# Kernel optimization log

Hardware: AMD Instinct MI355X
Metric: run time of the kernel (lower is better)

The kernel has to match this reference:

```python
import jax, jax.numpy as jnp
import numpy as np

N, E, D, H, ED = 50000, 600000, 128, 2, 5
C = D // H  # per-head channels = 64


def _lin(k, fan_in, fan_out):
    return jax.random.normal(k, (fan_out, fan_in), jnp.float32) / np.sqrt(fan_in)


def setup_inputs() -> dict:
    key = jax.random.key(0)
    ks = jax.random.split(key, 12)
    return {
        "x": jax.random.normal(ks[0], (N, D), jnp.float32),
        "edge_index": jax.random.randint(ks[1], (2, E), 0, N, dtype=jnp.int32),
        "edge_attr": jax.random.normal(ks[2], (E, ED), jnp.float32),
        "Wq": _lin(ks[3], D, D), "bq": jnp.zeros((D,), jnp.float32),
        "Wk": _lin(ks[4], D, D), "bk": jnp.zeros((D,), jnp.float32),
        "Wv": _lin(ks[5], D, D), "bv": jnp.zeros((D,), jnp.float32),
        "We": _lin(ks[6], ED, D),                       # lin_edge, bias=False in PyG
        "Wskip": _lin(ks[7], D, D), "bskip": jnp.zeros((D,), jnp.float32),
        "Wbeta": _lin(ks[8], 3 * D, 1),                 # lin_beta, bias=False
        "Wproj": _lin(ks[9], D, D), "bproj": jnp.zeros((D,), jnp.float32),
    }


def reference(x, edge_index, edge_attr, Wq, bq, Wk, bk, Wv, bv, We,
              Wskip, bskip, Wbeta, Wproj, bproj):
    src, dst = edge_index[0], edge_index[1]
    # node projections -> [N, H, C]
    q = (x @ Wq.T + bq).reshape(N, H, C)
    k = (x @ Wk.T + bk).reshape(N, H, C)
    v = (x @ Wv.T + bv).reshape(N, H, C)
    e = (edge_attr @ We.T).reshape(E, H, C)
    # gather per-edge, fold in edge features
    kj = k[src] + e                                   # [E, H, C]
    vj = v[src] + e                                   # [E, H, C]
    alpha = (q[dst] * kj).sum(-1) / np.sqrt(C)        # [E, H]
    # segment softmax over edges grouped by dst node
    amax = jax.ops.segment_max(alpha, dst, num_segments=N)   # [N, H]
    ex = jnp.exp(alpha - amax[dst])
    denom = jax.ops.segment_sum(ex, dst, num_segments=N)     # [N, H]
    w = ex / denom[dst]                               # [E, H]
    # scatter-aggregate weighted values, concat heads
    out = jax.ops.segment_sum(vj * w[:, :, None], dst, num_segments=N).reshape(N, D)
    # beta-gated skip connection
    x_r = x @ Wskip.T + bskip
    beta = jax.nn.sigmoid(jnp.concatenate([out, x_r, out - x_r], axis=-1) @ Wbeta.T)  # [N,1]
    out = beta * x_r + (1.0 - beta) * out
    # outer projection (dropout is identity in eval)
    return out @ Wproj.T + bproj
```

## Files before the change

kernel.cpp:

```cpp
#include <hip/hip_runtime.h>
#include <stdint.h>
#include <math.h>

#define D 128
#define EDIM 5

typedef __attribute__((ext_vector_type(8))) short bf16x8;
typedef __attribute__((ext_vector_type(4))) float f32x4;

__device__ __forceinline__ ushort f2b(float f) {
  union { float f; uint u; } v; v.f = f;
  uint u = v.u;
  return (ushort)((u + 0x7fff + ((u >> 16) & 1)) >> 16);
}
__device__ __forceinline__ float blo(uint u) {
  union { uint u; float f; } v; v.u = u << 16; return v.f;
}
__device__ __forceinline__ float bhi(uint u) {
  union { uint u; float f; } v; v.u = u & 0xffff0000u; return v.f;
}


__global__ void zero_int_kernel(int* __restrict__ p, int n) {
  int i = blockIdx.x * blockDim.x + threadIdx.x;
  if (i < n) p[i] = 0;
}

__global__ void hist_kernel(const int* __restrict__ ei, int* __restrict__ deg, int E) {
  int e = blockIdx.x * blockDim.x + threadIdx.x;
  if (e < E) atomicAdd(&deg[ei[(size_t)E + e]], 1);
}

__global__ __launch_bounds__(256) void scan_p1(const int* __restrict__ deg,
                                               int* __restrict__ off,
                                               int* __restrict__ blockSum, int n4) {
  __shared__ int waveTot[4];
  int idx = blockIdx.x * 256 + threadIdx.x;
  int4 v = make_int4(0, 0, 0, 0);
  if (idx < n4) v = ((const int4*)deg)[idx];
  int c0 = v.x, c1 = c0 + v.y, c2 = c1 + v.z, c3 = c2 + v.w;
  int tot = c3;
  int lane = threadIdx.x & 63, w = threadIdx.x >> 6;
  int incl = tot;
#pragma unroll
  for (int ofs = 1; ofs < 64; ofs <<= 1) {
    int t = __shfl_up(incl, ofs, 64);
    if (lane >= ofs) incl += t;
  }
  if (lane == 63) waveTot[w] = incl;
  __syncthreads();
  int wbase = 0;
  for (int i = 0; i < w; ++i) wbase += waveTot[i];
  int excl = wbase + incl - tot;
  if (idx < n4) {
    int4 o;
    o.x = excl; o.y = excl + c0; o.z = excl + c1; o.w = excl + c2;
    ((int4*)off)[idx] = o;
  }
  if (threadIdx.x == 255) blockSum[blockIdx.x] = wbase + incl;
}

__global__ void scan_p2(const int* __restrict__ blockSum, int* __restrict__ blockBase,
                        int* __restrict__ off_last, int nb) {
  int lane = threadIdx.x;
  int v = (lane < nb) ? blockSum[lane] : 0;
  int incl = v;
#pragma unroll
  for (int ofs = 1; ofs < 64; ofs <<= 1) {
    int t = __shfl_up(incl, ofs, 64);
    if (lane >= ofs) incl += t;
  }
  if (lane < nb) blockBase[lane] = incl - v;
  if (lane == 63) *off_last = incl;
}

__global__ __launch_bounds__(256) void scan_p3(int* __restrict__ off,
                                               const int* __restrict__ blockBase,
                                               int* __restrict__ cursor, int n4) {
  int idx = blockIdx.x * 256 + threadIdx.x;
  if (idx >= n4) return;
  int b = blockBase[blockIdx.x];
  int4 v = ((int4*)off)[idx];
  v.x += b; v.y += b; v.z += b; v.w += b;
  ((int4*)off)[idx] = v;
  ((int4*)cursor)[idx] = make_int4(0, 0, 0, 0);
}

__global__ void scatter_kernel(const int* __restrict__ ei, const float* __restrict__ ea,
                               const int* __restrict__ off, int* __restrict__ cursor,
                               int* __restrict__ ssrc, uint4* __restrict__ easrt, int E) {
  int e = blockIdx.x * blockDim.x + threadIdx.x;
  if (e >= E) return;
  int dst = ei[(size_t)E + e];
  int pos = off[dst] + atomicAdd(&cursor[dst], 1);
  ssrc[pos] = ei[e];
  const float* p = ea + (size_t)e * EDIM;
  uint e0 = f2b(p[0]), e1 = f2b(p[1]), e2 = f2b(p[2]), e3 = f2b(p[3]), e4 = f2b(p[4]);
  easrt[pos] = make_uint4(e0 | (e1 << 16), e2 | (e3 << 16), e4, 0);
}

__global__ void cvt_w_kernel(const float* __restrict__ Wq, const float* __restrict__ Wk,
                             const float* __restrict__ Wv, const float* __restrict__ Wr,
                             const float* __restrict__ bq, const float* __restrict__ bk,
                             const float* __restrict__ bv, const float* __restrict__ br,
                             const float* __restrict__ We, const float* __restrict__ Wp,
                             ushort* __restrict__ Wcat, float* __restrict__ bcat,
                             ushort* __restrict__ Wpb) {
  int i = blockIdx.x * blockDim.x + threadIdx.x;
  if (i < 512 * D) {
    int r = i >> 7;
    float v;
    if (r < 128)      v = Wq[i] * 0.125f;
    else if (r < 256) v = Wk[i - 128 * D];
    else if (r < 384) v = Wv[i - 256 * D];
    else              v = Wr[i - 384 * D];
    Wcat[i] = f2b(v);
  } else if (i < 512 * D + 128 * D) {
    int ie = i - 512 * D;
    int r = ie >> 7, c = ie & 127;
    int h = r >> 3, j = r & 7;
    float v = 0.f;
    if (h < 2 && j < 5) {
      for (int d = 0; d < 64; ++d) {
        int dd = h * 64 + d;
        v += We[(size_t)dd * EDIM + j] * 0.125f * Wq[(size_t)dd * D + c];
      }
    }
    Wcat[(size_t)(512 + r) * D + c] = f2b(v);
  }
  if (i < D * D) Wpb[i] = f2b(Wp[i]);
  if (i < 512) {
    float v = (i < 128) ? bq[i] * 0.125f
            : (i < 256) ? bk[i - 128]
            : (i < 384) ? bv[i - 256] : br[i - 384];
    bcat[i] = v;
  } else if (i < 640) {
    int t = i - 512;
    int h = t >> 3, j = t & 7;
    float v = 0.f;
    if (h < 2 && j < 5) {
      for (int d = 0; d < 64; ++d) {
        int dd = h * 64 + d;
        v += bq[dd] * 0.125f * We[(size_t)dd * EDIM + j];
      }
    }
    bcat[i] = v;
  }
}

__global__ __launch_bounds__(256) void proj_gemm_kernel(
    const float* __restrict__ x, const ushort* __restrict__ Wcat,
    const float* __restrict__ bcat,
    ushort* __restrict__ q, ushort* __restrict__ kv, ushort* __restrict__ xr,
    float* __restrict__ qwe, int M)
{
  __shared__ __attribute__((aligned(16))) ushort As[64][128];
  __shared__ __attribute__((aligned(16))) ushort Bs[128][128];
  const int tid = threadIdx.x;
  const int rowBase = blockIdx.x * 64;

#pragma unroll
  for (int it = 0; it < 4; ++it) {
    int i = it * 256 + tid;
    int r = i >> 4, c = i & 15;
    int gr = rowBase + r;
    float4 a0 = make_float4(0.f, 0.f, 0.f, 0.f), a1 = a0;
    if (gr < M) {
      a0 = *(const float4*)(x + (size_t)gr * D + c * 8);
      a1 = *(const float4*)(x + (size_t)gr * D + c * 8 + 4);
    }
    uint4 w;
    w.x = (uint)f2b(a0.x) | ((uint)f2b(a0.y) << 16);
    w.y = (uint)f2b(a0.z) | ((uint)f2b(a0.w) << 16);
    w.z = (uint)f2b(a1.x) | ((uint)f2b(a1.y) << 16);
    w.w = (uint)f2b(a1.z) | ((uint)f2b(a1.w) << 16);
    *(uint4*)(&As[r][(c ^ (r & 7)) * 8]) = w;
  }

  const int lane = tid & 63;
  const int wave = tid >> 6;
  const int wm = (wave >> 1) * 32;
  const int wn = (wave & 1) * 64;
  const int lrow = lane & 15;
  const int kgrp = lane >> 4;
  const int orow = (lane >> 4) * 4;
  const int ocol = lane & 15;

  for (int cb = 0; cb < 5; ++cb) {
#pragma unroll
    for (int it = 0; it < 8; ++it) {
      int i = it * 256 + tid;
      int r = i >> 4, c = i & 15;
      uint4 bv4 = *(const uint4*)(Wcat + (size_t)(cb * 128 + r) * D + c * 8);
      *(uint4*)(&Bs[r][(c ^ (r & 7)) * 8]) = bv4;
    }
    __syncthreads();

    f32x4 acc[2][4] = {};
#pragma unroll
    for (int ks = 0; ks < 4; ++ks) {
      int chunk = ks * 4 + kgrp;
      bf16x8 a[2], b[4];
#pragma unroll
      for (int m = 0; m < 2; ++m) {
        int r = wm + m * 16 + lrow;
        a[m] = *(const bf16x8*)&As[r][(chunk ^ (r & 7)) * 8];
      }
#pragma unroll
      for (int n = 0; n < 4; ++n) {
        int r = wn + n * 16 + lrow;
        b[n] = *(const bf16x8*)&Bs[r][(chunk ^ (r & 7)) * 8];
      }
#pragma unroll
      for (int m = 0; m < 2; ++m)
#pragma unroll
        for (int n = 0; n < 4; ++n)
          acc[m][n] = __builtin_amdgcn_mfma_f32_16x16x32_bf16(a[m], b[n], acc[m][n], 0, 0, 0);
    }

#pragma unroll
    for (int m = 0; m < 2; ++m) {
#pragma unroll
      for (int n = 0; n < 4; ++n) {
        int col = cb * 128 + wn + n * 16 + ocol;
        float bi = bcat[col];
        int sel = col >> 7, c = col & 127;
#pragma unroll
        for (int ii = 0; ii < 4; ++ii) {
          int gr = rowBase + wm + m * 16 + orow + ii;
          if (gr >= M) continue;
          float v = acc[m][n][ii] + bi;
          if (sel == 0)      q[(size_t)gr * D + c] = f2b(v);
          else if (sel == 1) kv[(size_t)gr * 2 * D + c] = f2b(v);
          else if (sel == 2) kv[(size_t)gr * 2 * D + D + c] = f2b(v);
          else if (sel == 3) xr[(size_t)gr * D + c] = f2b(v);
          else if (c < 16)   qwe[(size_t)gr * 16 + c] = v;
        }
      }
    }
    __syncthreads();
  }
}

__global__ __launch_bounds__(256) void out_gemm_kernel(
    const ushort* __restrict__ g, const ushort* __restrict__ Wpb,
    const float* __restrict__ bp, float* __restrict__ out, int M)
{
  __shared__ __attribute__((aligned(16))) ushort As[64][128];
  __shared__ __attribute__((aligned(16))) ushort Bs[128][128];
  const int tid = threadIdx.x;
  const int rowBase = blockIdx.x * 64;

#pragma unroll
  for (int it = 0; it < 4; ++it) {
    int i = it * 256 + tid;
    int r = i >> 4, c = i & 15;
    int gr = rowBase + r;
    uint4 av = make_uint4(0, 0, 0, 0);
    if (gr < M) av = *(const uint4*)(g + (size_t)gr * D + c * 8);
    *(uint4*)(&As[r][(c ^ (r & 7)) * 8]) = av;
  }
#pragma unroll
  for (int it = 0; it < 8; ++it) {
    int i = it * 256 + tid;
    int r = i >> 4, c = i & 15;
    uint4 bv4 = *(const uint4*)(Wpb + (size_t)r * D + c * 8);
    *(uint4*)(&Bs[r][(c ^ (r & 7)) * 8]) = bv4;
  }
  __syncthreads();

  const int lane = tid & 63;
  const int wave = tid >> 6;
  const int wm = (wave >> 1) * 32;
  const int wn = (wave & 1) * 64;
  const int lrow = lane & 15;
  const int kgrp = lane >> 4;

  f32x4 acc[2][4] = {};
#pragma unroll
  for (int ks = 0; ks < 4; ++ks) {
    int chunk = ks * 4 + kgrp;
    bf16x8 a[2], b[4];
#pragma unroll
    for (int m = 0; m < 2; ++m) {
      int r = wm + m * 16 + lrow;
      a[m] = *(const bf16x8*)&As[r][(chunk ^ (r & 7)) * 8];
    }
#pragma unroll
    for (int n = 0; n < 4; ++n) {
      int r = wn + n * 16 + lrow;
      b[n] = *(const bf16x8*)&Bs[r][(chunk ^ (r & 7)) * 8];
    }
#pragma unroll
    for (int m = 0; m < 2; ++m)
#pragma unroll
      for (int n = 0; n < 4; ++n)
        acc[m][n] = __builtin_amdgcn_mfma_f32_16x16x32_bf16(a[m], b[n], acc[m][n], 0, 0, 0);
  }

  const int orow = (lane >> 4) * 4;
  const int ocol = lane & 15;
#pragma unroll
  for (int m = 0; m < 2; ++m) {
#pragma unroll
    for (int n = 0; n < 4; ++n) {
      int col = wn + n * 16 + ocol;
      float bi = bp[col];
#pragma unroll
      for (int ii = 0; ii < 4; ++ii) {
        int gr = rowBase + wm + m * 16 + orow + ii;
        if (gr >= M) continue;
        out[(size_t)gr * D + col] = acc[m][n][ii] + bi;
      }
    }
  }
}

__global__ __launch_bounds__(256) void node_attn_kernel(
    const ushort* __restrict__ q, const ushort* __restrict__ kv,
    const ushort* __restrict__ xr, ushort* __restrict__ g,
    const float* __restrict__ qwe, const uint4* __restrict__ easrt,
    const float* __restrict__ We, const float* __restrict__ Wb,
    const int* __restrict__ off, const int* __restrict__ ssrc, int N)
{
  const int wid = threadIdx.x >> 6;
  const int lane = threadIdx.x & 63;
  const int node = blockIdx.x * 4 + wid;
  if (node >= N) return;
  const int grp = lane >> 4;
  const int i = lane & 15;
  const int di = i * 8;
  const int head = i >> 3;

  float qr[8];
  {
    uint4 qa = *(const uint4*)(q + (size_t)node * D + di);
    qr[0] = blo(qa.x); qr[1] = bhi(qa.x); qr[2] = blo(qa.y); qr[3] = bhi(qa.y);
    qr[4] = blo(qa.z); qr[5] = bhi(qa.z); qr[6] = blo(qa.w); qr[7] = bhi(qa.w);
  }
  float qw[5];
  {
    const float* qp = qwe + (size_t)node * 16 + head * 8;
    float4 t = *(const float4*)qp;
    qw[0] = t.x; qw[1] = t.y; qw[2] = t.z; qw[3] = t.w; qw[4] = qp[4];
  }

  const int beg = off[node], end = off[node + 1];
  float m = -INFINITY, s = 0.f;
  float o[8] = {0.f, 0.f, 0.f, 0.f, 0.f, 0.f, 0.f, 0.f};
  float wea[5] = {0.f, 0.f, 0.f, 0.f, 0.f};

  if (beg < end) {
    int p0 = beg + grp;
    bool valid_c = p0 < end;
    int pl = valid_c ? p0 : beg;
    int src_c = ssrc[pl];
    uint4 eau_c = easrt[pl];
    const ushort* kp0 = kv + (size_t)src_c * (2 * D);
    uint4 ku_c = *(const uint4*)(kp0 + di);
    uint4 vu_c = *(const uint4*)(kp0 + D + di);

    for (int pb = beg; pb < end; pb += 4) {
      int pn = pb + 4 + grp;
      bool valid_n = pn < end;
      int pln = valid_n ? pn : pl;
      int src_n = ssrc[pln];
      uint4 eau_n = easrt[pln];

      float ea0 = blo(eau_c.x), ea1 = bhi(eau_c.x), ea2 = blo(eau_c.y),
            ea3 = bhi(eau_c.y), ea4 = blo(eau_c.z);
      float part = qr[0] * blo(ku_c.x) + qr[1] * bhi(ku_c.x)
                 + qr[2] * blo(ku_c.y) + qr[3] * bhi(ku_c.y)
                 + qr[4] * blo(ku_c.z) + qr[5] * bhi(ku_c.z)
                 + qr[6] * blo(ku_c.w) + qr[7] * bhi(ku_c.w);
#pragma unroll
      for (int ofs = 1; ofs < 8; ofs <<= 1) part += __shfl_xor(part, ofs, 64);
      float eadot = qw[0] * ea0 + qw[1] * ea1 + qw[2] * ea2 + qw[3] * ea3 + qw[4] * ea4;
      float alpha = valid_c ? (part + eadot) : -INFINITY;

      const ushort* kpn = kv + (size_t)src_n * (2 * D);
      uint4 ku_n = *(const uint4*)(kpn + di);
      uint4 vu_n = *(const uint4*)(kpn + D + di);

      float v0 = blo(vu_c.x), v1 = bhi(vu_c.x), v2 = blo(vu_c.y), v3 = bhi(vu_c.y),
            v4 = blo(vu_c.z), v5 = bhi(vu_c.z), v6 = blo(vu_c.w), v7 = bhi(vu_c.w);

      if (__any(alpha > m + 8.f)) {
        float nm = fmaxf(m, alpha);
        float scale = (m > -1e30f) ? __expf(m - nm) : 0.f;
        float pw = (alpha > -1e30f) ? __expf(alpha - nm) : 0.f;
        m = nm;
        s = s * scale + pw;
        o[0] = o[0] * scale + pw * v0; o[1] = o[1] * scale + pw * v1;
        o[2] = o[2] * scale + pw * v2; o[3] = o[3] * scale + pw * v3;
        o[4] = o[4] * scale + pw * v4; o[5] = o[5] * scale + pw * v5;
        o[6] = o[6] * scale + pw * v6; o[7] = o[7] * scale + pw * v7;
        wea[0] = wea[0] * scale + pw * ea0; wea[1] = wea[1] * scale + pw * ea1;
        wea[2] = wea[2] * scale + pw * ea2; wea[3] = wea[3] * scale + pw * ea3;
        wea[4] = wea[4] * scale + pw * ea4;
      } else {
        float pw = (alpha > -1e30f) ? __expf(alpha - m) : 0.f;
        s += pw;
        o[0] += pw * v0; o[1] += pw * v1; o[2] += pw * v2; o[3] += pw * v3;
        o[4] += pw * v4; o[5] += pw * v5; o[6] += pw * v6; o[7] += pw * v7;
        wea[0] += pw * ea0; wea[1] += pw * ea1; wea[2] += pw * ea2;
        wea[3] += pw * ea3; wea[4] += pw * ea4;
      }

      ku_c = ku_n; vu_c = vu_n; eau_c = eau_n; valid_c = valid_n; pl = pln;
    }
  }

#pragma unroll
  for (int ofs = 16; ofs < 64; ofs <<= 1) {
    float m2 = __shfl_xor(m, ofs, 64);
    float s2 = __shfl_xor(s, ofs, 64);
    float o2[8], w2[5];
#pragma unroll
    for (int j = 0; j < 8; ++j) o2[j] = __shfl_xor(o[j], ofs, 64);
#pragma unroll
    for (int j = 0; j < 5; ++j) w2[j] = __shfl_xor(wea[j], ofs, 64);
    float nm = fmaxf(m, m2);
    float e1 = (m > -1e30f) ? __expf(m - nm) : 0.f;
    float e2 = (m2 > -1e30f) ? __expf(m2 - nm) : 0.f;
    s = s * e1 + s2 * e2;
#pragma unroll
    for (int j = 0; j < 8; ++j) o[j] = o[j] * e1 + o2[j] * e2;
#pragma unroll
    for (int j = 0; j < 5; ++j) wea[j] = wea[j] * e1 + w2[j] * e2;
    m = nm;
  }

  float inv = (s > 0.f) ? (1.f / s) : 0.f;
#pragma unroll
  for (int j = 0; j < 8; ++j) o[j] *= inv;
#pragma unroll
  for (int j = 0; j < 5; ++j) wea[j] *= inv;

  {
    const float* wp = We + (size_t)di * EDIM;
    float4 w[10];
#pragma unroll
    for (int t = 0; t < 10; ++t) w[t] = *(const float4*)(wp + 4 * t);
#pragma unroll
    for (int r = 0; r < 8; ++r)
#pragma unroll
      for (int j = 0; j < 5; ++j) {
        int idx = r * 5 + j;
        o[r] += wea[j] * ((const float*)&w[idx >> 2])[idx & 3];
      }
  }

  float xrv[8];
  {
    uint4 xa = *(const uint4*)(xr + (size_t)node * D + di);
    xrv[0] = blo(xa.x); xrv[1] = bhi(xa.x); xrv[2] = blo(xa.y); xrv[3] = bhi(xa.y);
    xrv[4] = blo(xa.z); xrv[5] = bhi(xa.z); xrv[6] = blo(xa.w); xrv[7] = bhi(xa.w);
  }
  float part = 0.f;
#pragma unroll
  for (int r = 0; r < 8; ++r) {
    float w1 = Wb[di + r] + Wb[256 + di + r];
    float w2 = Wb[128 + di + r] - Wb[256 + di + r];
    part += o[r] * w1 + xrv[r] * w2;
  }
#pragma unroll
  for (int ofs = 1; ofs < 16; ofs <<= 1) part += __shfl_xor(part, ofs, 64);
  float beta = 1.f / (1.f + __expf(-part));

  if (grp == 0) {
    uint pk[4];
#pragma unroll
    for (int r = 0; r < 4; ++r) {
      float g0 = beta * xrv[2 * r] + (1.f - beta) * o[2 * r];
      float g1 = beta * xrv[2 * r + 1] + (1.f - beta) * o[2 * r + 1];
      pk[r] = (uint)f2b(g0) | ((uint)f2b(g1) << 16);
    }
    *(uint4*)(g + (size_t)node * D + di) = make_uint4(pk[0], pk[1], pk[2], pk[3]);
  }
}


extern "C" void kernel_launch(void* const* d_in, const int* in_sizes, int n_in,
                              void* d_out, int out_size, void* d_ws, size_t ws_size,
                              hipStream_t stream)
{
  const float* x  = (const float*)d_in[0];
  const int*   ei = (const int*)d_in[1];
  const float* ea = (const float*)d_in[2];
  const float* Wq = (const float*)d_in[3];
  const float* bq = (const float*)d_in[4];
  const float* Wk = (const float*)d_in[5];
  const float* bk = (const float*)d_in[6];
  const float* Wv = (const float*)d_in[7];
  const float* bv = (const float*)d_in[8];
  const float* We = (const float*)d_in[9];
  const float* Wr = (const float*)d_in[10];
  const float* br = (const float*)d_in[11];
  const float* Wb = (const float*)d_in[12];
  const float* Wp = (const float*)d_in[13];
  const float* bp = (const float*)d_in[14];

  const int N = in_sizes[0] / D;
  const int E = in_sizes[1] / 2;
  float* out = (float*)d_out;

  char* ws = (char*)d_ws;
  size_t o = 0;
  auto alloc = [&](size_t bytes) -> void* {
    void* p = ws + o;
    o = (o + bytes + 255) & ~(size_t)255;
    return p;
  };
  ushort* q      = (ushort*)alloc((size_t)N * D * sizeof(ushort));
  ushort* kv     = (ushort*)alloc((size_t)N * 2 * D * sizeof(ushort));
  ushort* xr     = (ushort*)alloc((size_t)N * D * sizeof(ushort));
  ushort* g      = (ushort*)alloc((size_t)N * D * sizeof(ushort));
  float*  qwe    = (float*)alloc((size_t)N * 16 * sizeof(float));
  ushort* Wcat   = (ushort*)alloc((size_t)640 * D * sizeof(ushort));
  float*  bcat   = (float*)alloc(640 * sizeof(float));
  ushort* Wpb    = (ushort*)alloc((size_t)D * D * sizeof(ushort));
  int*    deg    = (int*)alloc((size_t)N * sizeof(int));
  int*    cursor = (int*)alloc((size_t)N * sizeof(int));
  int*    offs   = (int*)alloc((size_t)(N + 1) * sizeof(int));
  int*    ssrc   = (int*)alloc((size_t)E * sizeof(int));
  uint4*  easrt  = (uint4*)alloc((size_t)E * sizeof(uint4));
  int*    bsum   = (int*)alloc(64 * sizeof(int));
  int*    bbase  = (int*)alloc(64 * sizeof(int));

  const int n4 = N / 4;
  const int nb = (n4 + 255) / 256;

  zero_int_kernel<<<(N + 255) / 256, 256, 0, stream>>>(deg, N);
  hist_kernel<<<(E + 255) / 256, 256, 0, stream>>>(ei, deg, E);
  scan_p1<<<nb, 256, 0, stream>>>(deg, offs, bsum, n4);
  scan_p2<<<1, 64, 0, stream>>>(bsum, bbase, offs + N, nb);
  scan_p3<<<nb, 256, 0, stream>>>(offs, bbase, cursor, n4);
  scatter_kernel<<<(E + 255) / 256, 256, 0, stream>>>(ei, ea, offs, cursor, ssrc, easrt, E);

  cvt_w_kernel<<<(512 * D + 128 * D + 255) / 256, 256, 0, stream>>>(
      Wq, Wk, Wv, Wr, bq, bk, bv, br, We, Wp, Wcat, bcat, Wpb);

  proj_gemm_kernel<<<(N + 63) / 64, 256, 0, stream>>>(x, Wcat, bcat, q, kv, xr, qwe, N);

  node_attn_kernel<<<(N + 3) / 4, 256, 0, stream>>>(q, kv, xr, g, qwe, easrt, We, Wb,
                                                    offs, ssrc, N);

  out_gemm_kernel<<<(N + 63) / 64, 256, 0, stream>>>(g, Wpb, bp, out, N);
}
```

Baseline: 241.2 us.

## Pack src into edge record, deepen gather prefetch, use exp2, trim GEMM tail

The source index is now packed into the unused fourth word of the sorted edge-attribute record, which removes the separate ssrc array and one dependent load per edge. The attention loop is unrolled three ways with rotating registers, so K/V gathers are prefetched two groups ahead and edge records three ahead. The softmax switches to exp2 by folding log2(e) into the Q scale, and the rescale threshold is adjusted to match. Separately, the degree zeroing is folded into the weight-convert kernel, and the projection GEMM skips the unused columns of its last column block. The costs are higher register pressure in the attention kernel and more duplicated loads at the tail of each segment.

```diff
diff --git a/kernel.cpp b/kernel.cpp
--- a/kernel.cpp
+++ b/kernel.cpp
@@ -4,9 +4,14 @@
 
 #define D 128
 #define EDIM 5
+#define QSCALE 0.1803368801111204f
 
 typedef __attribute__((ext_vector_type(8))) short bf16x8;
 typedef __attribute__((ext_vector_type(4))) float f32x4;
+
+__device__ __forceinline__ float fexp2(float x) {
+  return __builtin_amdgcn_exp2f(x);
+}
 
 __device__ __forceinline__ ushort f2b(float f) {
   union { float f; uint u; } v; v.f = f;
@@ -20,11 +25,6 @@
   union { uint u; float f; } v; v.u = u & 0xffff0000u; return v.f;
 }
 
-
-__global__ void zero_int_kernel(int* __restrict__ p, int n) {
-  int i = blockIdx.x * blockDim.x + threadIdx.x;
-  if (i < n) p[i] = 0;
-}
 
 __global__ void hist_kernel(const int* __restrict__ ei, int* __restrict__ deg, int E) {
   int e = blockIdx.x * blockDim.x + threadIdx.x;
@@ -88,15 +88,14 @@
 
 __global__ void scatter_kernel(const int* __restrict__ ei, const float* __restrict__ ea,
                                const int* __restrict__ off, int* __restrict__ cursor,
-                               int* __restrict__ ssrc, uint4* __restrict__ easrt, int E) {
+                               uint4* __restrict__ easrt, int E) {
   int e = blockIdx.x * blockDim.x + threadIdx.x;
   if (e >= E) return;
   int dst = ei[(size_t)E + e];
   int pos = off[dst] + atomicAdd(&cursor[dst], 1);
-  ssrc[pos] = ei[e];
   const float* p = ea + (size_t)e * EDIM;
   uint e0 = f2b(p[0]), e1 = f2b(p[1]), e2 = f2b(p[2]), e3 = f2b(p[3]), e4 = f2b(p[4]);
-  easrt[pos] = make_uint4(e0 | (e1 << 16), e2 | (e3 << 16), e4, 0);
+  easrt[pos] = make_uint4(e0 | (e1 << 16), e2 | (e3 << 16), e4, (uint)ei[e]);
 }
 
 __global__ void cvt_w_kernel(const float* __restrict__ Wq, const float* __restrict__ Wk,
@@ -105,12 +104,13 @@
                              const float* __restrict__ bv, const float* __restrict__ br,
                              const float* __restrict__ We, const float* __restrict__ Wp,
                              ushort* __restrict__ Wcat, float* __restrict__ bcat,
-                             ushort* __restrict__ Wpb) {
+                             ushort* __restrict__ Wpb, int* __restrict__ deg, int N) {
   int i = blockIdx.x * blockDim.x + threadIdx.x;
+  if (i < N) deg[i] = 0;
   if (i < 512 * D) {
     int r = i >> 7;
     float v;
-    if (r < 128)      v = Wq[i] * 0.125f;
+    if (r < 128)      v = Wq[i] * QSCALE;
     else if (r < 256) v = Wk[i - 128 * D];
     else if (r < 384) v = Wv[i - 256 * D];
     else              v = Wr[i - 384 * D];
@@ -123,14 +123,14 @@
     if (h < 2 && j < 5) {
       for (int d = 0; d < 64; ++d) {
         int dd = h * 64 + d;
-        v += We[(size_t)dd * EDIM + j] * 0.125f * Wq[(size_t)dd * D + c];
+        v += We[(size_t)dd * EDIM + j] * QSCALE * Wq[(size_t)dd * D + c];
       }
     }
     Wcat[(size_t)(512 + r) * D + c] = f2b(v);
   }
   if (i < D * D) Wpb[i] = f2b(Wp[i]);
   if (i < 512) {
-    float v = (i < 128) ? bq[i] * 0.125f
+    float v = (i < 128) ? bq[i] * QSCALE
             : (i < 256) ? bk[i - 128]
             : (i < 384) ? bv[i - 256] : br[i - 384];
     bcat[i] = v;
@@ -141,7 +141,7 @@
     if (h < 2 && j < 5) {
       for (int d = 0; d < 64; ++d) {
         int dd = h * 64 + d;
-        v += bq[dd] * 0.125f * We[(size_t)dd * EDIM + j];
+        v += bq[dd] * QSCALE * We[(size_t)dd * EDIM + j];
       }
     }
     bcat[i] = v;
@@ -191,6 +191,7 @@
     for (int it = 0; it < 8; ++it) {
       int i = it * 256 + tid;
       int r = i >> 4, c = i & 15;
+      if (cb == 4 && r >= 16) continue;
       uint4 bv4 = *(const uint4*)(Wcat + (size_t)(cb * 128 + r) * D + c * 8);
       *(uint4*)(&Bs[r][(c ^ (r & 7)) * 8]) = bv4;
     }
@@ -214,14 +215,17 @@
 #pragma unroll
       for (int m = 0; m < 2; ++m)
 #pragma unroll
-        for (int n = 0; n < 4; ++n)
+        for (int n = 0; n < 4; ++n) {
+          if (cb == 4 && (wn + n * 16) >= 16) continue;
           acc[m][n] = __builtin_amdgcn_mfma_f32_16x16x32_bf16(a[m], b[n], acc[m][n], 0, 0, 0);
+        }
     }
 
 #pragma unroll
     for (int m = 0; m < 2; ++m) {
 #pragma unroll
       for (int n = 0; n < 4; ++n) {
+        if (cb == 4 && (wn + n * 16) >= 16) continue;
         int col = cb * 128 + wn + n * 16 + ocol;
         float bi = bcat[col];
         int sel = col >> 7, c = col & 127;
@@ -321,7 +325,7 @@
     const ushort* __restrict__ xr, ushort* __restrict__ g,
     const float* __restrict__ qwe, const uint4* __restrict__ easrt,
     const float* __restrict__ We, const float* __restrict__ Wb,
-    const int* __restrict__ off, const int* __restrict__ ssrc, int N)
+    const int* __restrict__ off, int N)
 {
   const int wid = threadIdx.x >> 6;
   const int lane = threadIdx.x & 63;
@@ -351,64 +355,74 @@
   float wea[5] = {0.f, 0.f, 0.f, 0.f, 0.f};
 
   if (beg < end) {
-    int p0 = beg + grp;
-    bool valid_c = p0 < end;
-    int pl = valid_c ? p0 : beg;
-    int src_c = ssrc[pl];
-    uint4 eau_c = easrt[pl];
-    const ushort* kp0 = kv + (size_t)src_c * (2 * D);
-    uint4 ku_c = *(const uint4*)(kp0 + di);
-    uint4 vu_c = *(const uint4*)(kp0 + D + di);
-
-    for (int pb = beg; pb < end; pb += 4) {
-      int pn = pb + 4 + grp;
-      bool valid_n = pn < end;
-      int pln = valid_n ? pn : pl;
-      int src_n = ssrc[pln];
-      uint4 eau_n = easrt[pln];
-
-      float ea0 = blo(eau_c.x), ea1 = bhi(eau_c.x), ea2 = blo(eau_c.y),
-            ea3 = bhi(eau_c.y), ea4 = blo(eau_c.z);
-      float part = qr[0] * blo(ku_c.x) + qr[1] * bhi(ku_c.x)
-                 + qr[2] * blo(ku_c.y) + qr[3] * bhi(ku_c.y)
-                 + qr[4] * blo(ku_c.z) + qr[5] * bhi(ku_c.z)
-                 + qr[6] * blo(ku_c.w) + qr[7] * bhi(ku_c.w);
-#pragma unroll
-      for (int ofs = 1; ofs < 8; ofs <<= 1) part += __shfl_xor(part, ofs, 64);
-      float eadot = qw[0] * ea0 + qw[1] * ea1 + qw[2] * ea2 + qw[3] * ea3 + qw[4] * ea4;
-      float alpha = valid_c ? (part + eadot) : -INFINITY;
-
-      const ushort* kpn = kv + (size_t)src_n * (2 * D);
-      uint4 ku_n = *(const uint4*)(kpn + di);
-      uint4 vu_n = *(const uint4*)(kpn + D + di);
-
-      float v0 = blo(vu_c.x), v1 = bhi(vu_c.x), v2 = blo(vu_c.y), v3 = bhi(vu_c.y),
-            v4 = blo(vu_c.z), v5 = bhi(vu_c.z), v6 = blo(vu_c.w), v7 = bhi(vu_c.w);
-
-      if (__any(alpha > m + 8.f)) {
-        float nm = fmaxf(m, alpha);
-        float scale = (m > -1e30f) ? __expf(m - nm) : 0.f;
-        float pw = (alpha > -1e30f) ? __expf(alpha - nm) : 0.f;
-        m = nm;
-        s = s * scale + pw;
-        o[0] = o[0] * scale + pw * v0; o[1] = o[1] * scale + pw * v1;
-        o[2] = o[2] * scale + pw * v2; o[3] = o[3] * scale + pw * v3;
-        o[4] = o[4] * scale + pw * v4; o[5] = o[5] * scale + pw * v5;
-        o[6] = o[6] * scale + pw * v6; o[7] = o[7] * scale + pw * v7;
-        wea[0] = wea[0] * scale + pw * ea0; wea[1] = wea[1] * scale + pw * ea1;
-        wea[2] = wea[2] * scale + pw * ea2; wea[3] = wea[3] * scale + pw * ea3;
-        wea[4] = wea[4] * scale + pw * ea4;
-      } else {
-        float pw = (alpha > -1e30f) ? __expf(alpha - m) : 0.f;
-        s += pw;
-        o[0] += pw * v0; o[1] += pw * v1; o[2] += pw * v2; o[3] += pw * v3;
-        o[4] += pw * v4; o[5] += pw * v5; o[6] += pw * v6; o[7] += pw * v7;
-        wea[0] += pw * ea0; wea[1] += pw * ea1; wea[2] += pw * ea2;
-        wea[3] += pw * ea3; wea[4] += pw * ea4;
-      }
-
-      ku_c = ku_n; vu_c = vu_n; eau_c = eau_n; valid_c = valid_n; pl = pln;
-    }
+    const int em1 = end - 1;
+    const int p0 = beg + grp;
+    uint4 e0 = easrt[min(p0, em1)];
+    uint4 e1 = easrt[min(p0 + 4, em1)];
+    uint4 e2 = easrt[min(p0 + 8, em1)];
+    const ushort* kp_;
+    kp_ = kv + (size_t)e0.w * (2 * D);
+    uint4 k0 = *(const uint4*)(kp_ + di), v0 = *(const uint4*)(kp_ + D + di);
+    kp_ = kv + (size_t)e1.w * (2 * D);
+    uint4 k1 = *(const uint4*)(kp_ + di), v1 = *(const uint4*)(kp_ + D + di);
+    uint4 k2v = k0, v2v = v0;
+
+#define ATT_STEP(PB, eA, eC, kA, vA, kC, vC)                                   \
+    {                                                                          \
+      int p = (PB) + grp;                                                      \
+      bool valid = p < end;                                                    \
+            \
+      const ushort* kpn = kv + (size_t)(eC).w * (2 * D);                       \
+      (kC) = *(const uint4*)(kpn + di);                                        \
+      (vC) = *(const uint4*)(kpn + D + di);                                    \
+                  \
+      float ea0 = blo((eA).x), ea1 = bhi((eA).x), ea2 = blo((eA).y),           \
+            ea3 = bhi((eA).y), ea4 = blo((eA).z);                              \
+      (eA) = easrt[min(p + 12, em1)];                                          \
+                                                      \
+      float part = qr[0] * blo((kA).x) + qr[1] * bhi((kA).x)                   \
+                 + qr[2] * blo((kA).y) + qr[3] * bhi((kA).y)                   \
+                 + qr[4] * blo((kA).z) + qr[5] * bhi((kA).z)                   \
+                 + qr[6] * blo((kA).w) + qr[7] * bhi((kA).w);                  \
+      part += __shfl_xor(part, 1, 64);                                         \
+      part += __shfl_xor(part, 2, 64);                                         \
+      part += __shfl_xor(part, 4, 64);                                         \
+      float eadot = qw[0] * ea0 + qw[1] * ea1 + qw[2] * ea2 + qw[3] * ea3      \
+                  + qw[4] * ea4;                                               \
+      float alpha = valid ? (part + eadot) : -INFINITY;                        \
+      float vv0 = blo((vA).x), vv1 = bhi((vA).x), vv2 = blo((vA).y),           \
+            vv3 = bhi((vA).y), vv4 = blo((vA).z), vv5 = bhi((vA).z),           \
+            vv6 = blo((vA).w), vv7 = bhi((vA).w);                              \
+      if (__any(alpha > m + 11.5f)) {                                          \
+        float nm = fmaxf(m, alpha);                                            \
+        float scale = (m > -1e30f) ? fexp2(m - nm) : 0.f;                      \
+        float pw = valid ? fexp2(alpha - nm) : 0.f;                            \
+        m = nm;                                                                \
+        s = s * scale + pw;                                                    \
+        o[0] = o[0] * scale + pw * vv0; o[1] = o[1] * scale + pw * vv1;        \
+        o[2] = o[2] * scale + pw * vv2; o[3] = o[3] * scale + pw * vv3;        \
+        o[4] = o[4] * scale + pw * vv4; o[5] = o[5] * scale + pw * vv5;        \
+        o[6] = o[6] * scale + pw * vv6; o[7] = o[7] * scale + pw * vv7;        \
+        wea[0] = wea[0] * scale + pw * ea0; wea[1] = wea[1] * scale + pw * ea1;\
+        wea[2] = wea[2] * scale + pw * ea2; wea[3] = wea[3] * scale + pw * ea3;\
+        wea[4] = wea[4] * scale + pw * ea4;                                    \
+      } else {                                                                 \
+        float pw = valid ? fexp2(alpha - m) : 0.f;                             \
+        s += pw;                                                               \
+        o[0] += pw * vv0; o[1] += pw * vv1; o[2] += pw * vv2;                  \
+        o[3] += pw * vv3; o[4] += pw * vv4; o[5] += pw * vv5;                  \
+        o[6] += pw * vv6; o[7] += pw * vv7;                                    \
+        wea[0] += pw * ea0; wea[1] += pw * ea1; wea[2] += pw * ea2;            \
+        wea[3] += pw * ea3; wea[4] += pw * ea4;                                \
+      }                                                                        \
+    }
+
+    for (int pb = beg; pb < end; pb += 12) {
+      ATT_STEP(pb,     e0, e2, k0, v0, k2v, v2v)
+      ATT_STEP(pb + 4, e1, e0, k1, v1, k0, v0)
+      ATT_STEP(pb + 8, e2, e1, k2v, v2v, k1, v1)
+    }
+#undef ATT_STEP
   }
 
 #pragma unroll
@@ -421,13 +435,13 @@
 #pragma unroll
     for (int j = 0; j < 5; ++j) w2[j] = __shfl_xor(wea[j], ofs, 64);
     float nm = fmaxf(m, m2);
-    float e1 = (m > -1e30f) ? __expf(m - nm) : 0.f;
-    float e2 = (m2 > -1e30f) ? __expf(m2 - nm) : 0.f;
-    s = s * e1 + s2 * e2;
-#pragma unroll
-    for (int j = 0; j < 8; ++j) o[j] = o[j] * e1 + o2[j] * e2;
-#pragma unroll
-    for (int j = 0; j < 5; ++j) wea[j] = wea[j] * e1 + w2[j] * e2;
+    float e1m = (m > -1e30f) ? fexp2(m - nm) : 0.f;
+    float e2m = (m2 > -1e30f) ? fexp2(m2 - nm) : 0.f;
+    s = s * e1m + s2 * e2m;
+#pragma unroll
+    for (int j = 0; j < 8; ++j) o[j] = o[j] * e1m + o2[j] * e2m;
+#pragma unroll
+    for (int j = 0; j < 5; ++j) wea[j] = wea[j] * e1m + w2[j] * e2m;
     m = nm;
   }
 
@@ -523,7 +537,6 @@
   int*    deg    = (int*)alloc((size_t)N * sizeof(int));
   int*    cursor = (int*)alloc((size_t)N * sizeof(int));
   int*    offs   = (int*)alloc((size_t)(N + 1) * sizeof(int));
-  int*    ssrc   = (int*)alloc((size_t)E * sizeof(int));
   uint4*  easrt  = (uint4*)alloc((size_t)E * sizeof(uint4));
   int*    bsum   = (int*)alloc(64 * sizeof(int));
   int*    bbase  = (int*)alloc(64 * sizeof(int));
@@ -531,20 +544,19 @@
   const int n4 = N / 4;
   const int nb = (n4 + 255) / 256;
 
-  zero_int_kernel<<<(N + 255) / 256, 256, 0, stream>>>(deg, N);
+  cvt_w_kernel<<<(512 * D + 128 * D + 255) / 256, 256, 0, stream>>>(
+      Wq, Wk, Wv, Wr, bq, bk, bv, br, We, Wp, Wcat, bcat, Wpb, deg, N);
+
   hist_kernel<<<(E + 255) / 256, 256, 0, stream>>>(ei, deg, E);
   scan_p1<<<nb, 256, 0, stream>>>(deg, offs, bsum, n4);
   scan_p2<<<1, 64, 0, stream>>>(bsum, bbase, offs + N, nb);
   scan_p3<<<nb, 256, 0, stream>>>(offs, bbase, cursor, n4);
-  scatter_kernel<<<(E + 255) / 256, 256, 0, stream>>>(ei, ea, offs, cursor, ssrc, easrt, E);
-
-  cvt_w_kernel<<<(512 * D + 128 * D + 255) / 256, 256, 0, stream>>>(
-      Wq, Wk, Wv, Wr, bq, bk, bv, br, We, Wp, Wcat, bcat, Wpb);
+  scatter_kernel<<<(E + 255) / 256, 256, 0, stream>>>(ei, ea, offs, cursor, easrt, E);
 
   proj_gemm_kernel<<<(N + 63) / 64, 256, 0, stream>>>(x, Wcat, bcat, q, kv, xr, qwe, N);
 
   node_attn_kernel<<<(N + 3) / 4, 256, 0, stream>>>(q, kv, xr, g, qwe, easrt, We, Wb,
-                                                    offs, ssrc, N);
+                                                    offs, N);
 
   out_gemm_kernel<<<(N + 63) / 64, 256, 0, stream>>>(g, Wpb, bp, out, N);
 }
```

After: 215.4 us. 1.12x faster.
